# Optimization experiments

Hardware: AMD Instinct MI355X
Metric: run time of the kernel (lower is better)

Reference implementation:

```python
import jax, jax.numpy as jnp
import numpy as np

HEAD = 64
EPS = 1e-5

def _cbr(x, W, gamma, beta, mean, var):
    # 1x1 conv (no bias) + BatchNorm2d (eval mode, running stats) + ReLU
    y = jnp.einsum('nchw,oc->nohw', x, W)
    scale = gamma * jax.lax.rsqrt(var + EPS)
    shift = beta - mean * scale
    return jax.nn.relu(y * scale[None, :, None, None] + shift[None, :, None, None])

def setup_inputs() -> dict:
    key = jax.random.key(0)
    ks = jax.random.split(key, 8)
    B, C, H, W = 1024, 512, 8, 8
    IC, P2 = C // 2, H * W
    d = {}
    d['query'] = jax.random.normal(ks[0], (B, C, H, W), jnp.float32)
    d['context'] = jax.random.normal(ks[1], (B, C, H, W), jnp.float32)
    d['pm_W'] = jax.random.normal(ks[2], (HEAD, P2, P2), jnp.float32) * 0.05
    d['pm_b'] = jax.random.normal(ks[3], (HEAD, P2), jnp.float32) * 0.02
    for i, (nm, o, ci) in enumerate([('g', IC, C), ('theta', IC, C), ('phi', IC, C), ('out', C, IC)]):
        k1, k2, k3, k4, k5 = jax.random.split(ks[4 + i], 5)
        d[nm + '_W'] = jax.random.normal(k1, (o, ci), jnp.float32) * (1.0 / np.sqrt(ci).astype(np.float32))
        d[nm + '_gamma'] = jax.random.uniform(k2, (o,), jnp.float32, 0.5, 1.5)
        d[nm + '_beta'] = jax.random.normal(k3, (o,), jnp.float32) * 0.1
        d[nm + '_mean'] = jax.random.normal(k4, (o,), jnp.float32) * 0.1
        d[nm + '_var'] = jax.random.uniform(k5, (o,), jnp.float32, 0.5, 1.5)
    return d

def reference(query, context, pm_W, pm_b,
              g_W, g_gamma, g_beta, g_mean, g_var,
              theta_W, theta_gamma, theta_beta, theta_mean, theta_var,
              phi_W, phi_gamma, phi_beta, phi_mean, phi_var,
              out_W, out_gamma, out_beta, out_mean, out_var):
    n, c, h, w = context.shape
    p2 = h * w
    inter = g_W.shape[0]
    dim = inter // HEAD  # per-head channel dim
    # position mixing over spatial tokens, per head-chunk of channels
    ctx = context.reshape(n, c, p2)
    ctx_h = ctx.reshape(n, HEAD, c // HEAD, p2)
    # nn.Linear on last dim: y = x @ W.T + b
    mlp = jnp.einsum('nhcp,hqp->nhcq', ctx_h, pm_W) + pm_b[None, :, None, :]
    ctx = (ctx + mlp.reshape(n, c, p2)).reshape(n, c, h, w)
    # projections (conv1x1 + BN + ReLU), split inter channels head-major
    gx = _cbr(ctx, g_W, g_gamma, g_beta, g_mean, g_var).reshape(n, HEAD, dim, p2).transpose(0, 1, 3, 2)      # [n,H,p2,d]
    th = _cbr(query, theta_W, theta_gamma, theta_beta, theta_mean, theta_var).reshape(n, HEAD, dim, p2).transpose(0, 1, 3, 2)
    ph = _cbr(ctx, phi_W, phi_gamma, phi_beta, phi_mean, phi_var).reshape(n, HEAD, dim, p2)                   # [n,H,d,p2]
    # embedded_gaussian: scaled QK^T softmax, then @ V
    logits = jnp.einsum('nhqd,nhdk->nhqk', th, ph) * (1.0 / dim ** 0.5)
    attn = jax.nn.softmax(logits, axis=-1)
    y = jnp.einsum('nhqk,nhkd->nhqd', attn, gx)               # [n,H,p2,d]
    y = y.transpose(0, 1, 3, 2).reshape(n, inter, h, w)        # head-major channel merge
    return query + _cbr(y, out_W, out_gamma, out_beta, out_mean, out_var)
```

## Files before the change

### kernel.cpp

```cpp
#include <hip/hip_runtime.h>
#include <stdint.h>


typedef short bf16x8 __attribute__((ext_vector_type(8)));
typedef float f32x4 __attribute__((ext_vector_type(4)));

#define MFMA16(a, b, c) __builtin_amdgcn_mfma_f32_16x16x32_bf16((a), (b), (c), 0, 0, 0)

#define WS_W     0u
#define WS_BN    1048576u
#define WS_PMW   1058816u
#define WS_CTX2  2097152u
#define WS_THQ   69206016u
#define WS_YHM   WS_CTX2

__device__ __forceinline__ unsigned short f2bf(float f) {
    union { float f; unsigned int i; } v; v.f = f;
    unsigned int r = v.i + 0x7fffu + ((v.i >> 16) & 1u);
    return (unsigned short)(r >> 16);
}
__device__ __forceinline__ unsigned cvtpk(float lo, float hi) {
    unsigned r;
    asm("v_cvt_pk_bf16_f32 %0, %1, %2" : "=v"(r) : "v"(lo), "v"(hi));
    return r;
}

__global__ __launch_bounds__(256) void k0_prep(char* __restrict__ ws,
    const float* __restrict__ thW, const float* __restrict__ phW,
    const float* __restrict__ gW,  const float* __restrict__ outW,
    const float* __restrict__ pmW,
    const float* __restrict__ th_g, const float* __restrict__ th_b,
    const float* __restrict__ th_m, const float* __restrict__ th_v,
    const float* __restrict__ ph_g, const float* __restrict__ ph_b,
    const float* __restrict__ ph_m, const float* __restrict__ ph_v,
    const float* __restrict__ g_g,  const float* __restrict__ g_b,
    const float* __restrict__ g_m,  const float* __restrict__ g_v,
    const float* __restrict__ o_g,  const float* __restrict__ o_b,
    const float* __restrict__ o_m,  const float* __restrict__ o_v) {
    int i = blockIdx.x * 256 + threadIdx.x;
    if (i < 524288) {
        int mat = i >> 17, el = i & 131071;
        const float* src = (mat == 0) ? thW : (mat == 1) ? phW : (mat == 2) ? gW : outW;
        ((unsigned short*)ws)[mat * 131072 + el] = f2bf(src[el]);
    } else if (i < 786432) {
        int el = i - 524288;
        ((unsigned short*)(ws + WS_PMW))[el] = f2bf(pmW[el]);
    } else if (i < 786432 + 2560) {
        int j = i - 786432;
        float* bn = (float*)(ws + WS_BN);
        float v;
        if (j < 256)        { int c = j;        v = th_g[c] * rsqrtf(th_v[c] + 1e-5f); }
        else if (j < 512)   { int c = j - 256;  float s = th_g[c] * rsqrtf(th_v[c] + 1e-5f); v = th_b[c] - th_m[c] * s; }
        else if (j < 768)   { int c = j - 512;  v = ph_g[c] * rsqrtf(ph_v[c] + 1e-5f); }
        else if (j < 1024)  { int c = j - 768;  float s = ph_g[c] * rsqrtf(ph_v[c] + 1e-5f); v = ph_b[c] - ph_m[c] * s; }
        else if (j < 1280)  { int c = j - 1024; v = g_g[c] * rsqrtf(g_v[c] + 1e-5f); }
        else if (j < 1536)  { int c = j - 1280; float s = g_g[c] * rsqrtf(g_v[c] + 1e-5f); v = g_b[c] - g_m[c] * s; }
        else if (j < 2048)  { int c = j - 1536; v = o_g[c] * rsqrtf(o_v[c] + 1e-5f); }
        else                { int c = j - 2048; float s = o_g[c] * rsqrtf(o_v[c] + 1e-5f); v = o_b[c] - o_m[c] * s; }
        bn[j] = v;
    }
}

__global__ __launch_bounds__(256) void k1_posmix(const float* __restrict__ ctx,
                                                 const float* __restrict__ pm_b,
                                                 char* __restrict__ ws) {
    __shared__ __align__(16) unsigned short stg[2 * 64 * 136];
    const unsigned short* pmw = (const unsigned short*)(ws + WS_PMW);
    unsigned short* ctx2 = (unsigned short*)(ws + WS_CTX2);
    int t = threadIdx.x, w = t >> 6, l = t & 63, g = l >> 4, li = l & 15;
    int n0 = (blockIdx.x >> 2) * 2;
    int r = blockIdx.x & 3;
    int ni = li >> 3, cc = li & 7;

#pragma unroll 2
    for (int hi = 0; hi < 4; ++hi) {
        int h = r * 16 + w * 4 + hi;
        const float* arow = ctx + (size_t)(n0 + ni) * 32768 + (size_t)(h * 8 + cc) * 64;
        bf16x8 a[2];
#pragma unroll
        for (int ks = 0; ks < 2; ++ks) {
            float4 f0 = *(const float4*)(arow + ks * 32 + g * 8);
            float4 f1 = *(const float4*)(arow + ks * 32 + g * 8 + 4);
            bf16x8 av;
            av[0] = (short)f2bf(f0.x); av[1] = (short)f2bf(f0.y);
            av[2] = (short)f2bf(f0.z); av[3] = (short)f2bf(f0.w);
            av[4] = (short)f2bf(f1.x); av[5] = (short)f2bf(f1.y);
            av[6] = (short)f2bf(f1.z); av[7] = (short)f2bf(f1.w);
            a[ks] = av;
        }
#pragma unroll
        for (int nt = 0; nt < 4; ++nt) {
            int q = nt * 16 + li;
            const unsigned short* br = pmw + h * 4096 + q * 64 + g * 8;
            bf16x8 b0 = *(const bf16x8*)br;
            bf16x8 b1 = *(const bf16x8*)(br + 32);
            f32x4 acc = {0.f, 0.f, 0.f, 0.f};
            acc = MFMA16(a[0], b0, acc);
            acc = MFMA16(a[1], b1, acc);
            float pb = pm_b[h * 64 + q];
#pragma unroll
            for (int rr = 0; rr < 4; ++rr) {
                int row = 4 * g + rr; int n2 = row >> 3, c2 = row & 7;
                float resid = ctx[(size_t)(n0 + n2) * 32768 + (size_t)(h * 8 + c2) * 64 + q];
                stg[n2 * 8704 + q * 136 + (h - r * 16) * 8 + c2] = f2bf(acc[rr] + resid + pb);
            }
        }
    }
    __syncthreads();
#pragma unroll
    for (int it = 0; it < 8; ++it) {
        int ci = it * 256 + t;
        int n2 = ci >> 10, q = (ci >> 4) & 63, seg = ci & 15;
        uint4 v = *(const uint4*)&stg[n2 * 8704 + q * 136 + seg * 8];
        *(uint4*)(ctx2 + (size_t)(n0 + n2) * 32768 + (size_t)q * 512 + r * 128 + seg * 8) = v;
    }
}

__global__ __launch_bounds__(256) void k1q_transpose(const float* __restrict__ query,
                                                     unsigned short* __restrict__ qT) {
    __shared__ __align__(16) unsigned short stg[64 * 132];
    int n = blockIdx.x, t = threadIdx.x;
    const float* qn = query + (size_t)n * 32768;
    unsigned short* on = qT + (size_t)n * 32768;
#pragma unroll 1
    for (int cs = 0; cs < 4; ++cs) {
        const float* qs = qn + cs * 128 * 64;
#pragma unroll
        for (int it = 0; it < 8; ++it) {
            int ci = it * 256 + t;
            int q = ci & 63, c0 = (ci >> 6) * 4;
            float f0 = qs[(c0 + 0) * 64 + q];
            float f1 = qs[(c0 + 1) * 64 + q];
            float f2 = qs[(c0 + 2) * 64 + q];
            float f3 = qs[(c0 + 3) * 64 + q];
            uint2 pk;
            pk.x = (unsigned)f2bf(f0) | ((unsigned)f2bf(f1) << 16);
            pk.y = (unsigned)f2bf(f2) | ((unsigned)f2bf(f3) << 16);
            *(uint2*)&stg[q * 132 + c0] = pk;
        }
        __syncthreads();
#pragma unroll
        for (int it = 0; it < 8; ++it) {
            int ci = it * 256 + t;
            int q = ci >> 5, sg = ci & 31;
            uint2 v = *(const uint2*)&stg[q * 132 + sg * 4];
            *(uint2*)(on + (size_t)q * 512 + cs * 128 + sg * 4) = v;
        }
        __syncthreads();
    }
}

__global__ __launch_bounds__(256) void k2_proj(char* __restrict__ ws,
                                               const unsigned short* __restrict__ qT) {
    __shared__ __align__(16) unsigned short lds[24576];
    int bid = blockIdx.x;
    int c8 = bid & 7, m = bid >> 3;
    int np = c8 * 64 + m / 6, r6 = m % 6;
    int mat = r6 >> 1;
    int och0 = (r6 & 1) * 128;
    int n0 = np * 2;
    const unsigned short* W = (const unsigned short*)ws + (size_t)mat * 131072;
    const float* bnm = (const float*)(ws + WS_BN) + mat * 512;
    unsigned short* outp = (unsigned short*)(ws + WS_THQ + (size_t)mat * 33554432u);
    const unsigned short* X = (mat == 0) ? qT : (const unsigned short*)(ws + WS_CTX2);
    int t = threadIdx.x, w = t >> 6, l = t & 63, g = l >> 4, li = l & 15;
    int wr = w >> 1, wc = w & 1;

    float sc[4], sh[4];
#pragma unroll
    for (int nti = 0; nti < 4; ++nti) {
        int och = och0 + wc * 64 + nti * 16 + li;
        sc[nti] = bnm[och];
        sh[nti] = bnm[256 + och];
    }

    f32x4 acc[4][4];
#pragma unroll
    for (int mt = 0; mt < 4; ++mt)
#pragma unroll
        for (int nti = 0; nti < 4; ++nti) acc[mt][nti] = (f32x4){0.f, 0.f, 0.f, 0.f};

    auto STAGE = [&](int kt) {
        int s = kt % 3;
        unsigned short* Ab = lds + s * 4096;
        unsigned short* Bb = lds + 12288 + s * 4096;
#pragma unroll
        for (int it = 0; it < 2; ++it) {
            int ci = it * 256 + t;
            int row = ci >> 2, ch = ci & 3;
            int nn = n0 + (row >> 6), q = row & 63;
            const unsigned short* src = X + (size_t)nn * 32768 + (size_t)q * 512 + kt * 32 + ((ch ^ ((row >> 1) & 3)) << 3);
            __builtin_amdgcn_global_load_lds(
                (const __attribute__((address_space(1))) void*)src,
                (__attribute__((address_space(3))) void*)(Ab + ci * 8), 16, 0, 0);
        }
#pragma unroll
        for (int it = 0; it < 2; ++it) {
            int ci = it * 256 + t;
            int row = ci >> 2, ch = ci & 3;
            const unsigned short* src = W + (size_t)(och0 + row) * 512 + kt * 32 + ((ch ^ ((row >> 1) & 3)) << 3);
            __builtin_amdgcn_global_load_lds(
                (const __attribute__((address_space(1))) void*)src,
                (__attribute__((address_space(3))) void*)(Bb + ci * 8), 16, 0, 0);
        }
    };
    auto COMPUTE = [&](int s) {
        const char* Ab = (const char*)(lds + s * 4096);
        const char* Bb = (const char*)(lds + 12288 + s * 4096);
        bf16x8 a[4], b[4];
#pragma unroll
        for (int mt = 0; mt < 4; ++mt) {
            int row = wr * 64 + mt * 16 + li;
            a[mt] = *(const bf16x8*)(Ab + row * 64 + (((g ^ ((row >> 1) & 3))) << 4));
        }
#pragma unroll
        for (int nti = 0; nti < 4; ++nti) {
            int br = wc * 64 + nti * 16 + li;
            b[nti] = *(const bf16x8*)(Bb + br * 64 + (((g ^ ((br >> 1) & 3))) << 4));
        }
#pragma unroll
        for (int mt = 0; mt < 4; ++mt)
#pragma unroll
            for (int nti = 0; nti < 4; ++nti)
                acc[mt][nti] = MFMA16(a[mt], b[nti], acc[mt][nti]);
    };

    STAGE(0);
    STAGE(1);
#pragma unroll 1
    for (int kt = 0; kt < 16; ++kt) {
        if (kt == 15) { asm volatile("s_waitcnt vmcnt(0)" ::: "memory"); }
        else          { asm volatile("s_waitcnt vmcnt(4)" ::: "memory"); }
        __builtin_amdgcn_s_barrier();
        __builtin_amdgcn_sched_barrier(0);
        if (kt < 14) STAGE(kt + 2);
        COMPUTE(kt % 3);
    }
    __syncthreads();

    unsigned short* stg = lds;
    if (mat != 2) {
#pragma unroll
        for (int mt = 0; mt < 4; ++mt)
#pragma unroll
            for (int nti = 0; nti < 4; ++nti)
#pragma unroll
                for (int rr = 0; rr < 4; ++rr) {
                    int mrow = wr * 64 + mt * 16 + g * 4 + rr;
                    int ocl = wc * 64 + nti * 16 + li;
                    float v = fmaxf(acc[mt][nti][rr] * sc[nti] + sh[nti], 0.f);
                    stg[mrow * 132 + ocl] = f2bf(v);
                }
        __syncthreads();
#pragma unroll
        for (int it = 0; it < 8; ++it) {
            int ci = it * 256 + t;
            int s = ci >> 5, e = ci & 31;
            int nl = s >> 5, hl = s & 31;
            int q0 = e * 2;
            uint2 v0 = *(const uint2*)&stg[(nl * 64 + q0) * 132 + hl * 4];
            uint2 v1 = *(const uint2*)&stg[(nl * 64 + q0 + 1) * 132 + hl * 4];
            uint4 o; o.x = v0.x; o.y = v0.y; o.z = v1.x; o.w = v1.y;
            unsigned short* dst = outp + (size_t)(n0 + nl) * 16384 + (size_t)((och0 >> 2) + hl) * 256 + q0 * 4;
            *(uint4*)dst = o;
        }
    } else {
#pragma unroll
        for (int mt = 0; mt < 4; ++mt)
#pragma unroll
            for (int nti = 0; nti < 4; ++nti)
#pragma unroll
                for (int rr = 0; rr < 4; ++rr) {
                    int mrow = wr * 64 + mt * 16 + g * 4 + rr;
                    int ocl = wc * 64 + nti * 16 + li;
                    float v = fmaxf(acc[mt][nti][rr] * sc[nti] + sh[nti], 0.f);
                    stg[ocl * 136 + mrow] = f2bf(v);
                }
        __syncthreads();
#pragma unroll
        for (int it = 0; it < 8; ++it) {
            int ci = it * 256 + t;
            int nl = (ci >> 10) & 1, hl = (ci >> 5) & 31, dd = (ci >> 3) & 3, q8 = ci & 7;
            uint4 o = *(const uint4*)&stg[(hl * 4 + dd) * 136 + nl * 64 + q8 * 8];
            unsigned short* dst = outp + (size_t)(n0 + nl) * 16384 + (size_t)((och0 >> 2) + hl) * 256 + dd * 64 + q8 * 8;
            *(uint4*)dst = o;
        }
    }
}

__global__ __launch_bounds__(256) void k3_attn(char* __restrict__ ws) {
    __shared__ __align__(16) unsigned short plds[4][4096];
    int n = blockIdx.x >> 1, half = blockIdx.x & 1;
    const unsigned short* th = (const unsigned short*)(ws + WS_THQ) + (size_t)n * 16384;
    const unsigned short* ph = (const unsigned short*)(ws + WS_THQ + 33554432u) + (size_t)n * 16384;
    const unsigned short* gx = (const unsigned short*)(ws + WS_THQ + 67108864u) + (size_t)n * 16384;
    unsigned short* yout = (unsigned short*)(ws + WS_YHM) + (size_t)n * 16384;
    int t = threadIdx.x, w = t >> 6, l = t & 63, g = l >> 4, li = l & 15;
    unsigned short* pw = &plds[w][0];
    const float Cs = 0.72134752044f;
    f32x4 z4 = {0.f, 0.f, 0.f, 0.f};
    bool zz = (g == 0);
    union FU { uint4 u; bf16x8 v8; };

#pragma unroll 1
    for (int hi = 0; hi < 8; ++hi) {
        int h = half * 32 + w * 8 + hi;
        const unsigned short* th_h = th + h * 256;
        const unsigned short* ph_h = ph + h * 256;
        const unsigned short* gx_h = gx + h * 256;
        bf16x8 a[4], b[4];
#pragma unroll
        for (int mt = 0; mt < 4; ++mt) {
            uint2 v = *(const uint2*)(ph_h + (mt * 16 + li) * 4);
            FU f;
            f.u.x = zz ? v.x : 0u;
            f.u.y = zz ? v.y : 0u;
            f.u.z = 0u; f.u.w = 0u;
            a[mt] = f.v8;
        }
#pragma unroll
        for (int nt = 0; nt < 4; ++nt) {
            uint2 v = *(const uint2*)(th_h + (nt * 16 + li) * 4);
            FU f;
            f.u.x = v.x; f.u.y = v.y; f.u.z = 0u; f.u.w = 0u;
            b[nt] = f.v8;
        }
        f32x4 p[4][4];
#pragma unroll
        for (int mt = 0; mt < 4; ++mt)
#pragma unroll
            for (int nt = 0; nt < 4; ++nt) p[mt][nt] = MFMA16(a[mt], b[nt], z4);

        float rs[4];
#pragma unroll
        for (int nt = 0; nt < 4; ++nt) {
#pragma unroll
            for (int mt = 0; mt < 4; ++mt) {
                f32x4 tv = p[mt][nt] * Cs + (-46.0f);
                f32x4 ev;
                ev[0] = __builtin_amdgcn_exp2f(tv[0]);
                ev[1] = __builtin_amdgcn_exp2f(tv[1]);
                ev[2] = __builtin_amdgcn_exp2f(tv[2]);
                ev[3] = __builtin_amdgcn_exp2f(tv[3]);
                p[mt][nt] = ev;
            }
            f32x4 s4 = (p[0][nt] + p[1][nt]) + (p[2][nt] + p[3][nt]);
            float sum = (s4[0] + s4[1]) + (s4[2] + s4[3]);
            sum += __shfl_xor(sum, 16);
            sum += __shfl_xor(sum, 32);
            rs[nt] = __builtin_amdgcn_rcpf(sum);
        }

#pragma unroll
        for (int mt = 0; mt < 4; ++mt)
#pragma unroll
            for (int nt = 0; nt < 4; ++nt) {
                int q = nt * 16 + li;
                uint2 dv;
                dv.x = cvtpk(p[mt][nt][0], p[mt][nt][1]);
                dv.y = cvtpk(p[mt][nt][2], p[mt][nt][3]);
                int c16w = 2 * mt + (g >> 1);
                int byt = q * 128 + (((c16w ^ (q & 7)) << 4)) + ((g & 1) << 3);
                *(uint2*)((char*)pw + byt) = dv;
            }

        bf16x8 afr0 = *(const bf16x8*)(gx_h + (li & 3) * 64 + g * 8);
        bf16x8 afr1 = *(const bf16x8*)(gx_h + (li & 3) * 64 + 32 + g * 8);
        f32x4 yv[4];
#pragma unroll
        for (int qt = 0; qt < 4; ++qt) {
            int q = qt * 16 + li;
            bf16x8 b0 = *(const bf16x8*)((const char*)pw + q * 128 + (((g) ^ (q & 7)) << 4));
            bf16x8 b1 = *(const bf16x8*)((const char*)pw + q * 128 + (((4 + g) ^ (q & 7)) << 4));
            f32x4 acc = MFMA16(afr0, b0, z4);
            acc = MFMA16(afr1, b1, acc);
            yv[qt] = acc;
        }

        if (l < 16) {
#pragma unroll
            for (int qt = 0; qt < 4; ++qt) {
                float s = rs[qt];
                uint2 pk;
                pk.x = cvtpk(yv[qt][0] * s, yv[qt][1] * s);
                pk.y = cvtpk(yv[qt][2] * s, yv[qt][3] * s);
                *(uint2*)(yout + h * 256 + (qt * 16 + l) * 4) = pk;
            }
        }
    }
}

__global__ __launch_bounds__(256) void k4_out(const float* __restrict__ query,
                                              char* __restrict__ ws,
                                              float* __restrict__ out) {
    __shared__ __align__(16) unsigned short yA[64 * 256];
    int n = blockIdx.x >> 1, half = blockIdx.x & 1;
    const unsigned short* yQ = (const unsigned short*)(ws + WS_YHM) + (size_t)n * 16384;
    const unsigned short* W = (const unsigned short*)ws + (size_t)3 * 131072;
    const float* bn = (const float*)(ws + WS_BN) + 1536;
    int t = threadIdx.x, w = t >> 6, l = t & 63, g = l >> 4, li = l & 15;
    int ochb = half * 256;

#pragma unroll
    for (int it = 0; it < 8; ++it) {
        int ci = it * 256 + t;
        *(uint4*)((char*)yA + ci * 16) = *(const uint4*)(yQ + ci * 8);
    }
    __syncthreads();

    f32x4 acc[4][4];
#pragma unroll
    for (int mt = 0; mt < 4; ++mt)
#pragma unroll
        for (int nti = 0; nti < 4; ++nti) acc[mt][nti] = (f32x4){0.f, 0.f, 0.f, 0.f};

#pragma unroll 1
    for (int kt = 0; kt < 4; ++kt) {
        bf16x8 a[4][2];
#pragma unroll
        for (int mt = 0; mt < 4; ++mt) {
            int q = mt * 16 + li;
            const char* base = (const char*)yA;
            int c0 = kt * 8 + g, c1 = kt * 8 + 4 + g;
            union U { uint2 u[2]; bf16x8 v; };
            U u0, u1;
            u0.u[0] = *(const uint2*)(base + c0 * 1024 + q * 8);
            u0.u[1] = *(const uint2*)(base + c0 * 1024 + 512 + q * 8);
            u1.u[0] = *(const uint2*)(base + c1 * 1024 + q * 8);
            u1.u[1] = *(const uint2*)(base + c1 * 1024 + 512 + q * 8);
            a[mt][0] = u0.v;
            a[mt][1] = u1.v;
        }
#pragma unroll
        for (int nti = 0; nti < 4; ++nti) {
            int och = ochb + w * 64 + nti * 16 + li;
            const unsigned short* wr = W + (size_t)och * 256 + kt * 64 + g * 8;
            bf16x8 b0 = *(const bf16x8*)wr;
            bf16x8 b1 = *(const bf16x8*)(wr + 32);
#pragma unroll
            for (int mt = 0; mt < 4; ++mt) {
                acc[mt][nti] = MFMA16(a[mt][0], b0, acc[mt][nti]);
                acc[mt][nti] = MFMA16(a[mt][1], b1, acc[mt][nti]);
            }
        }
    }

#pragma unroll
    for (int nti = 0; nti < 4; ++nti) {
        int och = ochb + w * 64 + nti * 16 + li;
        float sc = bn[och], sb = bn[512 + och];
#pragma unroll
        for (int mt = 0; mt < 4; ++mt) {
            int q0 = mt * 16 + 4 * g;
            size_t idx = (size_t)n * 32768 + (size_t)och * 64 + q0;
            float4 qv = *(const float4*)(query + idx);
            float4 ov;
            ov.x = qv.x + fmaxf(acc[mt][nti][0] * sc + sb, 0.f);
            ov.y = qv.y + fmaxf(acc[mt][nti][1] * sc + sb, 0.f);
            ov.z = qv.z + fmaxf(acc[mt][nti][2] * sc + sb, 0.f);
            ov.w = qv.w + fmaxf(acc[mt][nti][3] * sc + sb, 0.f);
            *(float4*)(out + idx) = ov;
        }
    }
}

extern "C" void kernel_launch(void* const* d_in, const int* in_sizes, int n_in,
                              void* d_out, int out_size, void* d_ws, size_t ws_size,
                              hipStream_t stream) {
    (void)in_sizes; (void)n_in; (void)out_size; (void)ws_size;
    const float* query   = (const float*)d_in[0];
    const float* context = (const float*)d_in[1];
    const float* pm_W    = (const float*)d_in[2];
    const float* pm_b    = (const float*)d_in[3];
    const float* g_W     = (const float*)d_in[4];
    const float* g_g     = (const float*)d_in[5];
    const float* g_b     = (const float*)d_in[6];
    const float* g_m     = (const float*)d_in[7];
    const float* g_v     = (const float*)d_in[8];
    const float* th_W    = (const float*)d_in[9];
    const float* th_g    = (const float*)d_in[10];
    const float* th_b    = (const float*)d_in[11];
    const float* th_m    = (const float*)d_in[12];
    const float* th_v    = (const float*)d_in[13];
    const float* ph_W    = (const float*)d_in[14];
    const float* ph_g    = (const float*)d_in[15];
    const float* ph_b    = (const float*)d_in[16];
    const float* ph_m    = (const float*)d_in[17];
    const float* ph_v    = (const float*)d_in[18];
    const float* o_W     = (const float*)d_in[19];
    const float* o_g     = (const float*)d_in[20];
    const float* o_b     = (const float*)d_in[21];
    const float* o_m     = (const float*)d_in[22];
    const float* o_v     = (const float*)d_in[23];
    char* ws = (char*)d_ws;
    unsigned short* qT = (unsigned short*)d_out;

    k0_prep<<<3082, 256, 0, stream>>>(ws, th_W, ph_W, g_W, o_W, pm_W,
                                      th_g, th_b, th_m, th_v,
                                      ph_g, ph_b, ph_m, ph_v,
                                      g_g, g_b, g_m, g_v,
                                      o_g, o_b, o_m, o_v);
    k1_posmix<<<2048, 256, 0, stream>>>(context, pm_b, ws);
    k1q_transpose<<<1024, 256, 0, stream>>>(query, qT);
    k2_proj<<<3072, 256, 0, stream>>>(ws, qT);
    k3_attn<<<2048, 256, 0, stream>>>(ws);
    k4_out<<<2048, 256, 0, stream>>>(query, ws, (float*)d_out);
}
```

Baseline: 355.8 us.

## Load projection weights directly from global and double-buffer only activations in LDS

Only the activation tile stays in LDS staging, now double-buffered with a barrier every iteration. The weight operand is read straight from global memory into registers inside the compute step, and the triple-buffered pipeline with explicit waitcnt control is dropped. This cuts LDS use per block, which may raise occupancy. The cost is global weight loads sitting directly on the MFMA critical path with no prefetch, and a full synchronisation each k-step.

```diff
diff --git a/kernel.cpp b/kernel.cpp
--- a/kernel.cpp
+++ b/kernel.cpp
@@ -152,7 +152,7 @@
 
 __global__ __launch_bounds__(256) void k2_proj(char* __restrict__ ws,
                                                const unsigned short* __restrict__ qT) {
-    __shared__ __align__(16) unsigned short lds[24576];
+    __shared__ __align__(16) unsigned short lds[17408];
     int bid = blockIdx.x;
     int c8 = bid & 7, m = bid >> 3;
     int np = c8 * 64 + m / 6, r6 = m % 6;
@@ -180,10 +180,7 @@
 #pragma unroll
         for (int nti = 0; nti < 4; ++nti) acc[mt][nti] = (f32x4){0.f, 0.f, 0.f, 0.f};
 
-    auto STAGE = [&](int kt) {
-        int s = kt % 3;
-        unsigned short* Ab = lds + s * 4096;
-        unsigned short* Bb = lds + 12288 + s * 4096;
+    auto STAGE_A = [&](int kt, int pb) {
 #pragma unroll
         for (int it = 0; it < 2; ++it) {
             int ci = it * 256 + t;
@@ -192,51 +189,37 @@
             const unsigned short* src = X + (size_t)nn * 32768 + (size_t)q * 512 + kt * 32 + ((ch ^ ((row >> 1) & 3)) << 3);
             __builtin_amdgcn_global_load_lds(
                 (const __attribute__((address_space(1))) void*)src,
-                (__attribute__((address_space(3))) void*)(Ab + ci * 8), 16, 0, 0);
-        }
-#pragma unroll
-        for (int it = 0; it < 2; ++it) {
-            int ci = it * 256 + t;
-            int row = ci >> 2, ch = ci & 3;
-            const unsigned short* src = W + (size_t)(och0 + row) * 512 + kt * 32 + ((ch ^ ((row >> 1) & 3)) << 3);
-            __builtin_amdgcn_global_load_lds(
-                (const __attribute__((address_space(1))) void*)src,
-                (__attribute__((address_space(3))) void*)(Bb + ci * 8), 16, 0, 0);
+                (__attribute__((address_space(3))) void*)(lds + pb * 4096 + ci * 8), 16, 0, 0);
         }
     };
-    auto COMPUTE = [&](int s) {
-        const char* Ab = (const char*)(lds + s * 4096);
-        const char* Bb = (const char*)(lds + 12288 + s * 4096);
+    auto COMPUTE = [&](int kt, int pb) {
+        const char* Ab = (const char*)(lds + pb * 4096);
         bf16x8 a[4], b[4];
+#pragma unroll
+        for (int nti = 0; nti < 4; ++nti) {
+            int och = och0 + wc * 64 + nti * 16 + li;
+            b[nti] = *(const bf16x8*)(W + (size_t)och * 512 + kt * 32 + g * 8);
+        }
 #pragma unroll
         for (int mt = 0; mt < 4; ++mt) {
             int row = wr * 64 + mt * 16 + li;
             a[mt] = *(const bf16x8*)(Ab + row * 64 + (((g ^ ((row >> 1) & 3))) << 4));
         }
 #pragma unroll
-        for (int nti = 0; nti < 4; ++nti) {
-            int br = wc * 64 + nti * 16 + li;
-            b[nti] = *(const bf16x8*)(Bb + br * 64 + (((g ^ ((br >> 1) & 3))) << 4));
-        }
-#pragma unroll
         for (int mt = 0; mt < 4; ++mt)
 #pragma unroll
             for (int nti = 0; nti < 4; ++nti)
                 acc[mt][nti] = MFMA16(a[mt], b[nti], acc[mt][nti]);
     };
 
-    STAGE(0);
-    STAGE(1);
+    STAGE_A(0, 0);
+    __syncthreads();
 #pragma unroll 1
     for (int kt = 0; kt < 16; ++kt) {
-        if (kt == 15) { asm volatile("s_waitcnt vmcnt(0)" ::: "memory"); }
-        else          { asm volatile("s_waitcnt vmcnt(4)" ::: "memory"); }
-        __builtin_amdgcn_s_barrier();
-        __builtin_amdgcn_sched_barrier(0);
-        if (kt < 14) STAGE(kt + 2);
-        COMPUTE(kt % 3);
-    }
-    __syncthreads();
+        if (kt < 15) STAGE_A(kt + 1, (kt + 1) & 1);
+        COMPUTE(kt, kt & 1);
+        __syncthreads();
+    }
 
     unsigned short* stg = lds;
     if (mat != 2) {
```

New measurement: 410.3 us. 1.15x slower.
